# Kernel tuning notes

Measured on AMD Instinct MI355X. Metric: run time of the kernel, lower is better.

The kernel has to match this reference:

```python
import jax, jax.numpy as jnp
import numpy as np

ANG = float(np.deg2rad(20.0))  # max rotation/shear angle (rad)
MAX_T = 6.0                    # max translation (pixels)


def _affine_mats(random, Wc, Hc):
    # Faithful to TCR.forward: note tx==ty and r==hx==hy since all use the same `random`.
    tx = (2.0 * MAX_T) * random - MAX_T
    ty = (2.0 * MAX_T) * random - MAX_T
    r = (2.0 * ANG) * random - ANG
    z = jnp.ones_like(random)          # max_z == min_z == 1.0
    hx = (2.0 * ANG) * random - ANG
    hy = (2.0 * ANG) * random - ANG
    a = hx - r
    b = hy + r
    chx, chy = jnp.cos(hx), jnp.cos(hy)
    T11 = z * jnp.cos(a) / chx
    T12 = z * jnp.sin(a) / chx
    T13 = (Wc * chx - Wc * z * jnp.cos(a) + 2 * tx * z * jnp.cos(a)
           - Hc * z * jnp.sin(a) + 2 * ty * z * jnp.sin(a)) / (2 * chx)
    T21 = z * jnp.sin(b) / chy
    T22 = z * jnp.cos(b) / chy
    T23 = (Hc * chy - Wc * z * jnp.cos(b) + 2 * ty * z * jnp.cos(b)
           - Wc * z * jnp.sin(b) + 2 * tx * z * jnp.sin(b)) / (2 * chy)
    row0 = jnp.stack([T11, T12, T13], axis=-1)
    row1 = jnp.stack([T21, T22, T23], axis=-1)
    return jnp.stack([row0, row1], axis=1)  # (B, 2, 3)


def _bilinear_sample(img, sx, sy):
    # img (B,C,H,W); sx,sy (B,H,W) source pixel coords; zeros padding (grid_sample semantics).
    B, C, H, W = img.shape
    x0f = jnp.floor(sx)
    y0f = jnp.floor(sy)
    x0 = x0f.astype(jnp.int32)
    y0 = y0f.astype(jnp.int32)
    wx = (sx - x0f)[:, None]  # (B,1,H,W)
    wy = (sy - y0f)[:, None]
    imgf = img.reshape(B, C, H * W)

    def gather(yi, xi):
        valid = (yi >= 0) & (yi < H) & (xi >= 0) & (xi < W)
        idx = jnp.clip(yi, 0, H - 1) * W + jnp.clip(xi, 0, W - 1)
        idx = jnp.broadcast_to(idx.reshape(B, 1, H * W), (B, C, H * W))
        v = jnp.take_along_axis(imgf, idx, axis=2).reshape(B, C, H, W)
        return v * valid[:, None, :, :].astype(img.dtype)

    v00 = gather(y0, x0)
    v01 = gather(y0, x0 + 1)
    v10 = gather(y0 + 1, x0)
    v11 = gather(y0 + 1, x0 + 1)
    return (v00 * (1 - wx) * (1 - wy) + v01 * wx * (1 - wy)
            + v10 * (1 - wx) * wy + v11 * wx * wy)


def _warp_affine(img, T):
    # kornia.warp_affine with align_corners=True reduces to: dst(x,y) = src(T^{-1} [x,y,1]).
    B, C, H, W = img.shape
    a, b, c = T[:, 0, 0], T[:, 0, 1], T[:, 0, 2]
    d, e, f = T[:, 1, 0], T[:, 1, 1], T[:, 1, 2]
    det = a * e - b * d
    ia, ib = e / det, -b / det
    id_, ie = -d / det, a / det
    ic = -(ia * c + ib * f)
    if_ = -(id_ * c + ie * f)
    ys, xs = jnp.meshgrid(jnp.arange(H, dtype=img.dtype),
                          jnp.arange(W, dtype=img.dtype), indexing='ij')
    bc = lambda v: v[:, None, None]  # (B,) -> (B,1,1)
    sx = bc(ia) * xs + bc(ib) * ys + bc(ic)  # (B,H,W)
    sy = bc(id_) * xs + bc(ie) * ys + bc(if_)
    return _bilinear_sample(img, sx, sy)


def setup_inputs() -> dict:
    key = jax.random.key(0)
    k1, k2 = jax.random.split(key)
    img = jax.random.normal(k1, (64, 3, 256, 256), dtype=jnp.float32)
    random = jax.random.uniform(k2, (64,), dtype=jnp.float32)
    return {"img": img, "random": random}


def reference(img, random):
    # Original uses Wc = img.shape[2], Hc = img.shape[3] (NCHW); square so equivalent.
    Wc = img.shape[2]
    Hc = img.shape[3]
    T = _affine_mats(random, float(Wc), float(Hc))
    return _warp_affine(img, T)
```

## Files before the change

kernel.cpp:

```cpp
#include <hip/hip_runtime.h>
#include <math.h>

#define BATCH 64
#define CH 3
#define IMH 256
#define IMW 256
#define HW (IMH * IMW)
#define NXCD 8

#define NRMAX 132
#define XW 68
#define XW4 (XW / 4)

__device__ __forceinline__ int clampi(int v, int lo, int hi) {
    return min(max(v, lo), hi);
}

__global__ __launch_bounds__(256, 4) void TCR_52536039964687_warp(
    const float* __restrict__ img,
    const float* __restrict__ rnd,
    float* __restrict__ out) {
    __shared__ float lds[NRMAX * XW];

    int w = blockIdx.x;
    int xcd = w & (NXCD - 1);
    int t = w >> 3;
    int b = ((t >> 4) << 3) | xcd;
    int tile = t & 15;
    int X0 = (tile & 3) << 6;
    int Y0 = (tile >> 2) << 6;

    int tid = threadIdx.x;
    int dx = tid & 63;
    int qy = tid >> 6;

    const float r = rnd[b];
    const float ANG  = 0.34906585039886590f;
    const float ANG2 = 0.69813170079773179f;
    const float Wc = (float)IMH;
    const float Hc = (float)IMW;

    float tx  = 12.0f * r - 6.0f;
    float ty  = tx;
    float rho = ANG2 * r - ANG;

    float s = __sinf(rho);
    float c = __cosf(rho);
    float cb = 2.f * c * c - 1.f;
    float sb = 2.f * s * c;
    float rcb = 1.f / cb;

    float ic  = 0.5f * Wc * (1.f - c) - tx;
    float id_ = -sb * c * rcb;
    float ie  = c * rcb;
    float P   = 0.5f * (Wc * c - Wc + 2.f * tx);
    float Q   = 0.5f * (Hc * c - Wc * cb + 2.f * ty * cb - Wc * sb + 2.f * tx * sb);
    float if_ = (sb * P - Q) * rcb;

    float X0f = (float)X0, X1f = (float)(X0 + 63);
    float Y0f = (float)Y0, Y1f = (float)(Y0 + 63);
    float sxlo = fmaf(c, X0f, ic);
    int lxmin = clampi((int)floorf(sxlo), 0, IMW - 2);
    int axlo = lxmin & ~3;

    float g0 = fmaf(ie, Y0f, if_);
    float g1 = fmaf(ie, Y1f, if_);
    float syA = fmaf(id_, X0f, g0), syB = fmaf(id_, X1f, g0);
    float syC = fmaf(id_, X0f, g1), syD = fmaf(id_, X1f, g1);
    float symin = fminf(fminf(syA, syB), fminf(syC, syD));
    float symax = fmaxf(fmaxf(syA, syB), fmaxf(syC, syD));
    int rlo = clampi((int)floorf(symin), 0, IMH - 1);
    int rhi = clampi((int)floorf(symax) + 1, 0, IMH - 1);
    int NR = rhi - rlo + 1;

    float fx = (float)(X0 + dx);
    float sx = fmaf(c, fx, ic);
    float x0f = floorf(sx);
    int x0 = (int)x0f;
    float wx = sx - x0f;
    int lx = clampi(x0, 0, IMW - 2);
    float wl = (x0 == lx) ? (1.f - wx) : ((x0 == lx - 1) ? wx : 0.f);
    float wh = (x0 == lx) ? wx : ((x0 == lx + 1) ? (1.f - wx) : 0.f);
    int px = lx - axlo;

    int   a0[16], a1[16];
    float wy0[16], wy1[16];
    #pragma unroll
    for (int k = 0; k < 16; ++k) {
        float fy = (float)(Y0 + qy + 4 * k);
        float sy = fmaf(id_, fx, fmaf(ie, fy, if_));
        float y0f = floorf(sy);
        int y0 = (int)y0f;
        int y1 = y0 + 1;
        float wy = sy - y0f;
        wy0[k] = ((y0 >= 0) & (y0 < IMH)) ? (1.f - wy) : 0.f;
        wy1[k] = ((y1 >= 0) & (y1 < IMH)) ? wy : 0.f;
        a0[k] = (clampi(y0, 0, IMH - 1) - rlo) * XW + px;
        a1[k] = (clampi(y1, 0, IMH - 1) - rlo) * XW + px;
    }

    const float* ibase = img + (size_t)b * CH * HW;
    float* obase = out + (size_t)b * CH * HW + (Y0 + qy) * IMW + X0 + dx;
    int nq = NR * XW4;

    for (int ch = 0; ch < CH; ++ch) {
        const float* cbase = ibase + ch * HW;
        for (int e = tid; e < nq; e += 256) {
            unsigned ue = (unsigned)e;
            unsigned row = ue / XW4;
            unsigned q = ue - row * XW4;
            int gq = min(axlo + 4 * (int)q, IMW - 4);
            float4 v = *(const float4*)(cbase + (rlo + (int)row) * IMW + gq);
            *((float4*)&lds[row * XW + 4 * q]) = v;
        }
        __syncthreads();
        #pragma unroll
        for (int k = 0; k < 16; ++k) {
            float l00 = lds[a0[k]], l01 = lds[a0[k] + 1];
            float l10 = lds[a1[k]], l11 = lds[a1[k] + 1];
            float v = (l00 * wl + l01 * wh) * wy0[k]
                    + (l10 * wl + l11 * wh) * wy1[k];
            __builtin_nontemporal_store(v, obase + ch * HW + 4 * k * IMW);
        }
        __syncthreads();
    }
}

extern "C" void kernel_launch(void* const* d_in, const int* in_sizes, int n_in,
                              void* d_out, int out_size, void* d_ws, size_t ws_size,
                              hipStream_t stream) {
    const float* img = (const float*)d_in[0];
    const float* rnd = (const float*)d_in[1];
    float* out = (float*)d_out;
    (void)d_ws; (void)ws_size;

    hipLaunchKernelGGL(TCR_52536039964687_warp, dim3(BATCH * 16), dim3(256), 0, stream,
                       img, rnd, out);
}
```

Measured before the change: 26.07 us.

## Double-buffer LDS staging with register prefetch and halve tile height

```diff
diff --git a/kernel.cpp b/kernel.cpp
--- a/kernel.cpp
+++ b/kernel.cpp
@@ -8,27 +8,30 @@
 #define HW (IMH * IMW)
 #define NXCD 8
 
-#define NRMAX 132
+#define NRMAX 92
 #define XW 68
-#define XW4 (XW / 4)
+#define XW4 17
+#define LDSF (NRMAX * XW)
+#define NPF 7
 
 __device__ __forceinline__ int clampi(int v, int lo, int hi) {
     return min(max(v, lo), hi);
 }
 
-__global__ __launch_bounds__(256, 4) void TCR_52536039964687_warp(
+__global__ __launch_bounds__(256, 3) void TCR_52536039964687_warp(
     const float* __restrict__ img,
     const float* __restrict__ rnd,
     float* __restrict__ out) {
-    __shared__ float lds[NRMAX * XW];
+    __shared__ float bufA[LDSF];
+    __shared__ float bufB[LDSF];
 
     int w = blockIdx.x;
     int xcd = w & (NXCD - 1);
     int t = w >> 3;
-    int b = ((t >> 4) << 3) | xcd;
-    int tile = t & 15;
+    int b = ((t >> 5) << 3) | xcd;
+    int tile = t & 31;
     int X0 = (tile & 3) << 6;
-    int Y0 = (tile >> 2) << 6;
+    int Y0 = (tile >> 2) << 5;
 
     int tid = threadIdx.x;
     int dx = tid & 63;
@@ -58,7 +61,7 @@
     float if_ = (sb * P - Q) * rcb;
 
     float X0f = (float)X0, X1f = (float)(X0 + 63);
-    float Y0f = (float)Y0, Y1f = (float)(Y0 + 63);
+    float Y0f = (float)Y0, Y1f = (float)(Y0 + 31);
     float sxlo = fmaf(c, X0f, ic);
     int lxmin = clampi((int)floorf(sxlo), 0, IMW - 2);
     int axlo = lxmin & ~3;
@@ -72,6 +75,7 @@
     int rlo = clampi((int)floorf(symin), 0, IMH - 1);
     int rhi = clampi((int)floorf(symax) + 1, 0, IMH - 1);
     int NR = rhi - rlo + 1;
+    int nq = NR * XW4;
 
     float fx = (float)(X0 + dx);
     float sx = fmaf(c, fx, ic);
@@ -83,10 +87,10 @@
     float wh = (x0 == lx) ? wx : ((x0 == lx + 1) ? (1.f - wx) : 0.f);
     int px = lx - axlo;
 
-    int   a0[16], a1[16];
-    float wy0[16], wy1[16];
+    int   a0[8], a1[8];
+    float wy0[8], wy1[8];
     #pragma unroll
-    for (int k = 0; k < 16; ++k) {
+    for (int k = 0; k < 8; ++k) {
         float fy = (float)(Y0 + qy + 4 * k);
         float sy = fmaf(id_, fx, fmaf(ie, fy, if_));
         float y0f = floorf(sy);
@@ -101,29 +105,62 @@
 
     const float* ibase = img + (size_t)b * CH * HW;
     float* obase = out + (size_t)b * CH * HW + (Y0 + qy) * IMW + X0 + dx;
-    int nq = NR * XW4;
 
-    for (int ch = 0; ch < CH; ++ch) {
-        const float* cbase = ibase + ch * HW;
-        for (int e = tid; e < nq; e += 256) {
-            unsigned ue = (unsigned)e;
-            unsigned row = ue / XW4;
-            unsigned q = ue - row * XW4;
-            int gq = min(axlo + 4 * (int)q, IMW - 4);
-            float4 v = *(const float4*)(cbase + (rlo + (int)row) * IMW + gq);
-            *((float4*)&lds[row * XW + 4 * q]) = v;
-        }
-        __syncthreads();
-        #pragma unroll
-        for (int k = 0; k < 16; ++k) {
-            float l00 = lds[a0[k]], l01 = lds[a0[k] + 1];
-            float l10 = lds[a1[k]], l11 = lds[a1[k] + 1];
-            float v = (l00 * wl + l01 * wh) * wy0[k]
-                    + (l10 * wl + l11 * wh) * wy1[k];
-            __builtin_nontemporal_store(v, obase + ch * HW + 4 * k * IMW);
-        }
-        __syncthreads();
+    float4 pre[NPF];
+
+    #define PREFETCH(ch_) {                                                   \
+        const float* cbase = ibase + (ch_) * HW;                              \
+        _Pragma("unroll")                                                     \
+        for (int it = 0; it < NPF; ++it) {                                    \
+            int e = tid + it * 256;                                           \
+            if (e < nq) {                                                     \
+                unsigned row = (unsigned)e / XW4;                             \
+                int q = e - (int)row * XW4;                                   \
+                int gq = min(axlo + 4 * q, IMW - 4); \
+                pre[it] = *(const float4*)(cbase + (rlo + (int)row) * IMW + gq);\
+            }                                                                 \
+        }                                                                     \
     }
+
+    #define WRITE_STAGE(buf_) {                                               \
+        _Pragma("unroll")                                                     \
+        for (int it = 0; it < NPF; ++it) {                                    \
+            int e = tid + it * 256;                                           \
+            if (e < nq) {                                                     \
+                unsigned row = (unsigned)e / XW4;                             \
+                int q = e - (int)row * XW4;                                   \
+                *((float4*)&(buf_)[row * XW + 4 * q]) = pre[it];              \
+            }                                                                 \
+        }                                                                     \
+    }
+
+    #define SAMPLE(ch_, buf_) {                                               \
+        _Pragma("unroll")                                                     \
+        for (int k = 0; k < 8; ++k) {                                         \
+            float l00 = (buf_)[a0[k]], l01 = (buf_)[a0[k] + 1];               \
+            float l10 = (buf_)[a1[k]], l11 = (buf_)[a1[k] + 1];               \
+            float v = (l00 * wl + l01 * wh) * wy0[k]                          \
+                    + (l10 * wl + l11 * wh) * wy1[k];                         \
+            __builtin_nontemporal_store(v, obase + (ch_) * HW + 4 * k * IMW); \
+        }                                                                     \
+    }
+
+    PREFETCH(0);
+    WRITE_STAGE(bufA);
+    PREFETCH(1);
+    __syncthreads();
+    SAMPLE(0, bufA);
+    WRITE_STAGE(bufB);
+    PREFETCH(2);
+    __syncthreads();
+    SAMPLE(1, bufB);
+    WRITE_STAGE(bufA);
+    __syncthreads();
+    SAMPLE(2, bufA);
+
+    #undef PREFETCH
+    #undef WRITE_STAGE
+    #undef SAMPLE
 }
 
 extern "C" void kernel_launch(void* const* d_in, const int* in_sizes, int n_in,
@@ -134,6 +171,6 @@
     float* out = (float*)d_out;
     (void)d_ws; (void)ws_size;
 
-    hipLaunchKernelGGL(TCR_52536039964687_warp, dim3(BATCH * 16), dim3(256), 0, stream,
+    hipLaunchKernelGGL(TCR_52536039964687_warp, dim3(BATCH * 32), dim3(256), 0, stream,
                        img, rnd, out);
 }
```

New measurement: 45.04 us. 1.73x slower.

## Split channels across blocks and stage tiles with async global-to-LDS loads

Applied to the files above, without the earlier changes.

```diff
diff --git a/kernel.cpp b/kernel.cpp
--- a/kernel.cpp
+++ b/kernel.cpp
@@ -10,7 +10,11 @@
 
 #define NRMAX 132
 #define XW 68
-#define XW4 (XW / 4)
+#define XW4 17
+#define NQMAX 2304
+
+#define AS1 __attribute__((address_space(1)))
+#define AS3 __attribute__((address_space(3)))
 
 __device__ __forceinline__ int clampi(int v, int lo, int hi) {
     return min(max(v, lo), hi);
@@ -20,13 +24,17 @@
     const float* __restrict__ img,
     const float* __restrict__ rnd,
     float* __restrict__ out) {
-    __shared__ float lds[NRMAX * XW];
+    __shared__ float4 lds4[NQMAX];
+    float* lds = (float*)lds4;
 
     int w = blockIdx.x;
     int xcd = w & (NXCD - 1);
-    int t = w >> 3;
-    int b = ((t >> 4) << 3) | xcd;
-    int tile = t & 15;
+    unsigned t = (unsigned)w >> 3;
+    unsigned islot = t / 48u;
+    unsigned rem = t - islot * 48u;
+    int b = ((int)islot << 3) | xcd;
+    int ch = (int)(rem >> 4);
+    int tile = (int)(rem & 15u);
     int X0 = (tile & 3) << 6;
     int Y0 = (tile >> 2) << 6;
 
@@ -73,6 +81,21 @@
     int rhi = clampi((int)floorf(symax) + 1, 0, IMH - 1);
     int NR = rhi - rlo + 1;
 
+    {
+        const float* cbase = img + (size_t)b * CH * HW + ch * HW;
+        #pragma unroll
+        for (int it = 0; it < 9; ++it) {
+            int e = tid + it * 256;
+            unsigned row = (unsigned)e / XW4;
+            int q = e - (int)row * XW4;
+            int rr = min((int)row, NR - 1);
+            int gq = min(axlo + 4 * q, IMW - 4);
+            const float* gp = cbase + (rlo + rr) * IMW + gq;
+            __builtin_amdgcn_global_load_lds((const AS1 void*)gp,
+                                             (AS3 void*)&lds4[e], 16, 0, 0);
+        }
+    }
+
     float fx = (float)(X0 + dx);
     float sx = fmaf(c, fx, ic);
     float x0f = floorf(sx);
@@ -83,7 +106,7 @@
     float wh = (x0 == lx) ? wx : ((x0 == lx + 1) ? (1.f - wx) : 0.f);
     int px = lx - axlo;
 
-    int   a0[16], a1[16];
+    int   a01[16];
     float wy0[16], wy1[16];
     #pragma unroll
     for (int k = 0; k < 16; ++k) {
@@ -95,34 +118,24 @@
         float wy = sy - y0f;
         wy0[k] = ((y0 >= 0) & (y0 < IMH)) ? (1.f - wy) : 0.f;
         wy1[k] = ((y1 >= 0) & (y1 < IMH)) ? wy : 0.f;
-        a0[k] = (clampi(y0, 0, IMH - 1) - rlo) * XW + px;
-        a1[k] = (clampi(y1, 0, IMH - 1) - rlo) * XW + px;
+        int a0 = (clampi(y0, 0, IMH - 1) - rlo) * XW + px;
+        int a1 = (clampi(y1, 0, IMH - 1) - rlo) * XW + px;
+        a01[k] = a0 | (a1 << 16);
     }
 
-    const float* ibase = img + (size_t)b * CH * HW;
-    float* obase = out + (size_t)b * CH * HW + (Y0 + qy) * IMW + X0 + dx;
-    int nq = NR * XW4;
+    __syncthreads();
 
-    for (int ch = 0; ch < CH; ++ch) {
-        const float* cbase = ibase + ch * HW;
-        for (int e = tid; e < nq; e += 256) {
-            unsigned ue = (unsigned)e;
-            unsigned row = ue / XW4;
-            unsigned q = ue - row * XW4;
-            int gq = min(axlo + 4 * (int)q, IMW - 4);
-            float4 v = *(const float4*)(cbase + (rlo + (int)row) * IMW + gq);
-            *((float4*)&lds[row * XW + 4 * q]) = v;
-        }
-        __syncthreads();
-        #pragma unroll
-        for (int k = 0; k < 16; ++k) {
-            float l00 = lds[a0[k]], l01 = lds[a0[k] + 1];
-            float l10 = lds[a1[k]], l11 = lds[a1[k] + 1];
-            float v = (l00 * wl + l01 * wh) * wy0[k]
-                    + (l10 * wl + l11 * wh) * wy1[k];
-            __builtin_nontemporal_store(v, obase + ch * HW + 4 * k * IMW);
-        }
-        __syncthreads();
+    float* obase = out + (size_t)b * CH * HW + ch * HW
+                 + (Y0 + qy) * IMW + X0 + dx;
+    #pragma unroll
+    for (int k = 0; k < 16; ++k) {
+        int a0 = a01[k] & 0xffff;
+        int a1 = a01[k] >> 16;
+        float l00 = lds[a0], l01 = lds[a0 + 1];
+        float l10 = lds[a1], l11 = lds[a1 + 1];
+        float v = (l00 * wl + l01 * wh) * wy0[k]
+                + (l10 * wl + l11 * wh) * wy1[k];
+        __builtin_nontemporal_store(v, obase + 4 * k * IMW);
     }
 }
 
@@ -134,6 +147,6 @@
     float* out = (float*)d_out;
     (void)d_ws; (void)ws_size;
 
-    hipLaunchKernelGGL(TCR_52536039964687_warp, dim3(BATCH * 16), dim3(256), 0, stream,
-                       img, rnd, out);
+    hipLaunchKernelGGL(TCR_52536039964687_warp, dim3(BATCH * 16 * CH), dim3(256),
+                       0, stream, img, rnd, out);
 }
```

After: 24.10 us. -7.6%, faster.
